# Optimization experiments

Measured on AMD Instinct MI355X. Metric: run time of the kernel, lower is better.

Reference implementation:

```python
import jax, jax.numpy as jnp
import numpy as np

N_EMBED = 1024
N_HEADS = 16
HEAD_DIM = N_EMBED // N_HEADS


def setup_inputs() -> dict:
    key = jax.random.key(0)
    ks = jax.random.split(key, 5)
    x = jax.random.normal(ks[0], (4, 2048, N_EMBED), dtype=jnp.float32)
    # Linear params (torch nn.Linear: y = x @ W.T + b); store W as [in, out]
    s = 1.0 / np.sqrt(N_EMBED)
    W_attn = jax.random.uniform(ks[1], (N_EMBED, 3 * N_EMBED), minval=-s, maxval=s, dtype=jnp.float32)
    b_attn = jax.random.uniform(ks[2], (3 * N_EMBED,), minval=-s, maxval=s, dtype=jnp.float32)
    W_proj = jax.random.uniform(ks[3], (N_EMBED, N_EMBED), minval=-s, maxval=s, dtype=jnp.float32)
    b_proj = jax.random.uniform(ks[4], (N_EMBED,), minval=-s, maxval=s, dtype=jnp.float32)
    return {"x": x, "W_attn": W_attn, "b_attn": b_attn, "W_proj": W_proj, "b_proj": b_proj}


def reference(x, W_attn, b_attn, W_proj, b_proj):
    B, L, D = x.shape
    H, Hd = N_HEADS, HEAD_DIM
    qkv = x @ W_attn + b_attn  # [B, L, 3D]
    q, k, v = jnp.split(qkv, 3, axis=-1)
    q = q.reshape(B, L, H, Hd).transpose(0, 2, 1, 3)  # [B, H, L, Hd]
    k = k.reshape(B, L, H, Hd).transpose(0, 2, 1, 3)
    v = v.reshape(B, L, H, Hd).transpose(0, 2, 1, 3)
    scores = jnp.einsum('bhqd,bhkd->bhqk', q, k) / jnp.sqrt(jnp.float32(Hd))
    causal = jnp.tril(jnp.ones((L, L), dtype=bool))
    scores = jnp.where(causal[None, None], scores, -jnp.inf)
    probs = jax.nn.softmax(scores.astype(jnp.float32), axis=-1).astype(x.dtype)
    o = jnp.einsum('bhqk,bhkd->bhqd', probs, v)  # [B, H, L, Hd]
    o = o.transpose(0, 2, 1, 3).reshape(B, L, D)
    return o @ W_proj + b_proj
```

## Files before the change

kernel.cpp:

```cpp
#include <hip/hip_runtime.h>


typedef __attribute__((ext_vector_type(8))) short short8;
typedef __attribute__((ext_vector_type(4))) short s16x4;
typedef __attribute__((ext_vector_type(4))) float f32x4;

#define DEVI __device__ __forceinline__

constexpr int NE = 1024, NH = 16, NB = 4, L = 2048;
constexpr int M = NB * L;
constexpr int KD = 1024;

DEVI unsigned f2bf(float f) {
    union { float f; unsigned u; } v; v.f = f;
    unsigned u = v.u;
    u += 0x7fffu + ((u >> 16) & 1u);
    return u >> 16;
}

typedef const __attribute__((address_space(1))) void* gas_t;
typedef __attribute__((address_space(3))) void* las_t;
DEVI void gl_lds16(const void* g, void* l) {
    __builtin_amdgcn_global_load_lds((gas_t)g, (las_t)l, 16, 0, 0);
}

__global__ void k_f32_to_bf16(const float* __restrict__ in,
                              unsigned short* __restrict__ out, int n8) {
    int i = blockIdx.x * blockDim.x + threadIdx.x;
    if (i >= n8) return;
    const float4* p = (const float4*)in + (size_t)i * 2;
    float4 a = p[0], b = p[1];
    short8 r;
    r[0] = f2bf(a.x); r[1] = f2bf(a.y); r[2] = f2bf(a.z); r[3] = f2bf(a.w);
    r[4] = f2bf(b.x); r[5] = f2bf(b.y); r[6] = f2bf(b.z); r[7] = f2bf(b.w);
    ((short8*)out)[i] = r;
}

__global__ void k_transpose_bf16(const float* __restrict__ in,
                                 unsigned short* __restrict__ out, int R, int C) {
    __shared__ float t[32][33];
    int x = blockIdx.x * 32 + threadIdx.x;
    int y0 = blockIdx.y * 32;
#pragma unroll
    for (int i = 0; i < 4; i++)
        t[threadIdx.y + 8 * i][threadIdx.x] = in[(size_t)(y0 + threadIdx.y + 8 * i) * C + x];
    __syncthreads();
    int xo = y0 + threadIdx.x;
    int yo = blockIdx.x * 32 + threadIdx.y;
#pragma unroll
    for (int i = 0; i < 4; i++)
        out[(size_t)(yo + 8 * i) * R + xo] = f2bf(t[threadIdx.x][threadIdx.y + 8 * i]);
}

template <int MODE>
__global__ __launch_bounds__(256, 2)
void k_gemm(const unsigned short* __restrict__ A,
            const unsigned short* __restrict__ Bt,
            const float* __restrict__ bias,
            unsigned short* __restrict__ Qb,
            unsigned short* __restrict__ Kb,
            unsigned short* __restrict__ Vt,
            float* __restrict__ out) {
    __shared__ alignas(16) short As[128 * 64];
    __shared__ alignas(16) short Bs[128 * 64];
    const int tid = threadIdx.x;
    const int lane = tid & 63, wid = tid >> 6;
    const int quad = lane >> 4, l16 = lane & 15;
    const int wm = (wid >> 1) * 64, wn = (wid & 1) * 64;
    const int m0 = blockIdx.y * 128;
    const int n0 = blockIdx.x * 128;

    const int srow = lane >> 3;
    const int gseg = (lane & 7) ^ srow;

    f32x4 acc[4][4] = {};

    for (int kk = 0; kk < KD; kk += 64) {
        __syncthreads();
#pragma unroll
        for (int c = 0; c < 4; c++) {
            const int rbase = c * 32 + wid * 8;
            gl_lds16(&A[(size_t)(m0 + rbase + srow) * KD + kk + gseg * 8], &As[rbase * 64]);
            gl_lds16(&Bt[(size_t)(n0 + rbase + srow) * KD + kk + gseg * 8], &Bs[rbase * 64]);
        }
        __syncthreads();
#pragma unroll
        for (int kc = 0; kc < 2; kc++) {
            short8 af[4], bf[4];
#pragma unroll
            for (int t = 0; t < 4; t++) {
                const int Ra = wm + t * 16 + l16;
                af[t] = *(const short8*)&As[Ra * 64 + (((kc * 4 + quad) ^ (Ra & 7)) * 8)];
                const int Rb = wn + t * 16 + l16;
                bf[t] = *(const short8*)&Bs[Rb * 64 + (((kc * 4 + quad) ^ (Rb & 7)) * 8)];
            }
#pragma unroll
            for (int mt = 0; mt < 4; mt++)
#pragma unroll
                for (int nt = 0; nt < 4; nt++)
                    acc[mt][nt] = __builtin_amdgcn_mfma_f32_16x16x32_bf16(
                        af[mt], bf[nt], acc[mt][nt], 0, 0, 0);
        }
    }

#pragma unroll
    for (int nt = 0; nt < 4; nt++) {
        const int n = n0 + wn + nt * 16 + l16;
        const float bv = bias[n];
        if (MODE == 0) {
            const int sel = n >> 10;
            const int h = (n & 1023) >> 6;
            const int d = n & 63;
#pragma unroll
            for (int mt = 0; mt < 4; mt++)
#pragma unroll
                for (int r = 0; r < 4; r++) {
                    const int m = m0 + wm + mt * 16 + quad * 4 + r;
                    const int b = m >> 11, l = m & 2047;
                    const int bh = b * NH + h;
                    const float v = acc[mt][nt][r] + bv;
                    if (sel == 0)      Qb[(size_t)(bh * L + l) * 64 + d] = f2bf(v * 0.125f);
                    else if (sel == 1) Kb[(size_t)(bh * L + l) * 64 + d] = f2bf(v);
                    else               Vt[(size_t)(bh * 64 + d) * L + l] = f2bf(v);
                }
        } else {
#pragma unroll
            for (int mt = 0; mt < 4; mt++)
#pragma unroll
                for (int r = 0; r < 4; r++) {
                    const int m = m0 + wm + mt * 16 + quad * 4 + r;
                    out[(size_t)m * NE + n] = acc[mt][nt][r] + bv;
                }
        }
    }
}

__global__ __launch_bounds__(256, 2)
void k_attn(const unsigned short* __restrict__ Q,
            const unsigned short* __restrict__ Kb,
            const unsigned short* __restrict__ Vt,
            unsigned short* __restrict__ O) {
    __shared__ alignas(16) short smem[16896];
    short* Ks = smem;
    short* Vs = smem + 8192;
    short* Os = smem;

    const int tid = threadIdx.x;
    const int lane = tid & 63, wid = tid >> 6;
    const int quad = lane >> 4, l16 = lane & 15;
    const int bh = blockIdx.x;
    const int pr = blockIdx.y;
    const size_t base = (size_t)bh * L * 64;
    const int b = bh >> 4, h = bh & 15;

    const int srow = lane >> 3;
    const int gsegK = (lane & 7) ^ srow;

    for (int phase = 0; phase < 2; phase++) {
        const int qb = phase ? pr : 15 - pr;
        const int q0 = qb * 128 + wid * 32;

        short8 qf[2][2];
#pragma unroll
        for (int mt = 0; mt < 2; mt++)
#pragma unroll
            for (int dc = 0; dc < 2; dc++)
                qf[mt][dc] = *(const short8*)&Q[base + (size_t)(q0 + mt * 16 + l16) * 64 + dc * 32 + quad * 8];

        f32x4 o[2][4] = {};
        float lrow[2] = {0.f, 0.f};

        for (int kt = 0; kt <= qb; kt++) {
            __syncthreads();
#pragma unroll
            for (int c = 0; c < 4; c++) {
                const int rbase = c * 32 + wid * 8;
                gl_lds16(&Kb[base + (size_t)(kt * 128 + rbase + srow) * 64 + gsegK * 8],
                         &Ks[rbase * 64]);
            }
            short8 vtmp[4];
            const int vd = lane >> 4, vseg = lane & 15;
#pragma unroll
            for (int c = 0; c < 4; c++)
                vtmp[c] = *(const short8*)&Vt[base + (size_t)(c * 16 + wid * 4 + vd) * L + kt * 128 + vseg * 8];
#pragma unroll
            for (int c = 0; c < 4; c++)
                *(short8*)&Vs[(c * 16 + wid * 4 + vd) * 136 + vseg * 8] = vtmp[c];
            __syncthreads();

            const bool diag = (kt == qb);
            const int chunks = diag ? (wid + 1) : 4;

            for (int kc = 0; kc < chunks; kc++) {
                short8 kf[2][2];
#pragma unroll
                for (int j0 = 0; j0 < 2; j0++)
#pragma unroll
                    for (int dc = 0; dc < 2; dc++) {
                        const int R = kc * 32 + j0 * 16 + l16;
                        kf[j0][dc] = *(const short8*)&Ks[R * 64 + (((dc * 4 + quad) ^ (R & 7)) * 8)];
                    }
                f32x4 st[2][2];
#pragma unroll
                for (int mt = 0; mt < 2; mt++)
#pragma unroll
                    for (int j0 = 0; j0 < 2; j0++) {
                        f32x4 z = {};
                        z = __builtin_amdgcn_mfma_f32_16x16x32_bf16(kf[j0][0], qf[mt][0], z, 0, 0, 0);
                        z = __builtin_amdgcn_mfma_f32_16x16x32_bf16(kf[j0][1], qf[mt][1], z, 0, 0, 0);
                        st[mt][j0] = z;
                    }
                const bool dm = diag && (kc == wid);
                short8 pb[2];
#pragma unroll
                for (int mt = 0; mt < 2; mt++) {
                    float sum = 0.f;
#pragma unroll
                    for (int j0 = 0; j0 < 2; j0++)
#pragma unroll
                        for (int r = 0; r < 4; r++) {
                            float pe = __expf(st[mt][j0][r]);
                            if (dm) {
                                const int krel = j0 * 16 + quad * 4 + r;
                                const int qrel = mt * 16 + l16;
                                if (krel > qrel) pe = 0.f;
                            }
                            sum += pe;
                            pb[mt][j0 * 4 + r] = (short)f2bf(pe);
                        }
                    lrow[mt] += sum;
                }
#pragma unroll
                for (int dt = 0; dt < 4; dt++) {
                    const int va = (dt * 16 + l16) * 136 + kc * 32 + quad * 4;
                    s16x4 lo = *(const s16x4*)&Vs[va];
                    s16x4 hi = *(const s16x4*)&Vs[va + 16];
                    short8 vf = __builtin_shufflevector(lo, hi, 0, 1, 2, 3, 4, 5, 6, 7);
#pragma unroll
                    for (int mt = 0; mt < 2; mt++)
                        o[mt][dt] = __builtin_amdgcn_mfma_f32_16x16x32_bf16(
                            vf, pb[mt], o[mt][dt], 0, 0, 0);
                }
            }
        }

        float inv[2];
#pragma unroll
        for (int mt = 0; mt < 2; mt++) {
            float rs = lrow[mt];
            rs += __shfl_xor(rs, 16);
            rs += __shfl_xor(rs, 32);
            inv[mt] = 1.0f / rs;
        }

        __syncthreads();
#pragma unroll
        for (int mt = 0; mt < 2; mt++) {
            const int ql = wid * 32 + mt * 16 + l16;
#pragma unroll
            for (int dt = 0; dt < 4; dt++) {
                unsigned w0 = f2bf(o[mt][dt][0] * inv[mt]) | (f2bf(o[mt][dt][1] * inv[mt]) << 16);
                unsigned w1 = f2bf(o[mt][dt][2] * inv[mt]) | (f2bf(o[mt][dt][3] * inv[mt]) << 16);
                *(uint2*)&Os[ql * 72 + dt * 16 + quad * 4] = make_uint2(w0, w1);
            }
        }
        __syncthreads();
#pragma unroll
        for (int i = 0; i < 4; i++) {
            const int id = i * 256 + tid;
            const int row = id >> 3, seg = id & 7;
            short8 v = *(const short8*)&Os[row * 72 + seg * 8];
            const int q = qb * 128 + row;
            *(short8*)&O[(size_t)(b * L + q) * NE + h * 64 + seg * 8] = v;
        }
    }
}

extern "C" void kernel_launch(void* const* d_in, const int* in_sizes, int n_in,
                              void* d_out, int out_size, void* d_ws, size_t ws_size,
                              hipStream_t stream) {
    const float* x  = (const float*)d_in[0];
    const float* Wa = (const float*)d_in[1];
    const float* ba = (const float*)d_in[2];
    const float* Wp = (const float*)d_in[3];
    const float* bp = (const float*)d_in[4];
    float* out = (float*)d_out;

    char* ws = (char*)d_ws;
    unsigned short* xb  = (unsigned short*)(ws);
    unsigned short* WaT = (unsigned short*)(ws + (16u << 20));
    unsigned short* WpT = (unsigned short*)(ws + (22u << 20));
    unsigned short* Qb  = (unsigned short*)(ws + (24u << 20));
    unsigned short* Kb  = (unsigned short*)(ws + (40u << 20));
    unsigned short* Vt  = (unsigned short*)(ws + (56u << 20));

    k_f32_to_bf16<<<(M * NE / 8 + 255) / 256, 256, 0, stream>>>(x, xb, M * NE / 8);
    k_transpose_bf16<<<dim3(3 * NE / 32, NE / 32), dim3(32, 8), 0, stream>>>(Wa, WaT, NE, 3 * NE);
    k_transpose_bf16<<<dim3(NE / 32, NE / 32), dim3(32, 8), 0, stream>>>(Wp, WpT, NE, NE);

    k_gemm<0><<<dim3(3 * NE / 128, M / 128), 256, 0, stream>>>(xb, WaT, ba, Qb, Kb, Vt, nullptr);

    unsigned short* Ob = xb;
    k_attn<<<dim3(NB * NH, 8), 256, 0, stream>>>(Qb, Kb, Vt, Ob);

    k_gemm<1><<<dim3(NE / 128, M / 128), 256, 0, stream>>>(Ob, WpT, bp, nullptr, nullptr, nullptr, out);
}
```

Measured before the change: 267.7 us.

## Split attention to one q-block per workgroup, async swizzled V loads

```diff
diff --git a/kernel.cpp b/kernel.cpp
--- a/kernel.cpp
+++ b/kernel.cpp
@@ -16,6 +16,10 @@
     unsigned u = v.u;
     u += 0x7fffu + ((u >> 16) & 1u);
     return u >> 16;
+}
+DEVI unsigned pack_bf2(float lo, float hi) {
+    union { float f; unsigned u; } a, b; a.f = lo; b.f = hi;
+    return ((a.u + 0x8000u) >> 16) | ((b.u + 0x8000u) & 0xffff0000u);
 }
 
 typedef const __attribute__((address_space(1))) void* gas_t;
@@ -53,7 +57,7 @@
 }
 
 template <int MODE>
-__global__ __launch_bounds__(256, 2)
+__global__ __launch_bounds__(256, 4)
 void k_gemm(const unsigned short* __restrict__ A,
             const unsigned short* __restrict__ Bt,
             const float* __restrict__ bias,
@@ -135,12 +139,12 @@
     }
 }
 
-__global__ __launch_bounds__(256, 2)
+__global__ __launch_bounds__(256, 4)
 void k_attn(const unsigned short* __restrict__ Q,
             const unsigned short* __restrict__ Kb,
             const unsigned short* __restrict__ Vt,
             unsigned short* __restrict__ O) {
-    __shared__ alignas(16) short smem[16896];
+    __shared__ alignas(16) short smem[16384];
     short* Ks = smem;
     short* Vs = smem + 8192;
     short* Os = smem;
@@ -149,130 +153,136 @@
     const int lane = tid & 63, wid = tid >> 6;
     const int quad = lane >> 4, l16 = lane & 15;
     const int bh = blockIdx.x;
-    const int pr = blockIdx.y;
+    const int qb = 15 - (int)blockIdx.y;
+    const int q0 = qb * 128 + wid * 32;
     const size_t base = (size_t)bh * L * 64;
     const int b = bh >> 4, h = bh & 15;
 
-    const int srow = lane >> 3;
-    const int gsegK = (lane & 7) ^ srow;
-
-    for (int phase = 0; phase < 2; phase++) {
-        const int qb = phase ? pr : 15 - pr;
-        const int q0 = qb * 128 + wid * 32;
-
-        short8 qf[2][2];
-#pragma unroll
-        for (int mt = 0; mt < 2; mt++)
-#pragma unroll
-            for (int dc = 0; dc < 2; dc++)
-                qf[mt][dc] = *(const short8*)&Q[base + (size_t)(q0 + mt * 16 + l16) * 64 + dc * 32 + quad * 8];
-
-        f32x4 o[2][4] = {};
-        float lrow[2] = {0.f, 0.f};
-
-        for (int kt = 0; kt <= qb; kt++) {
-            __syncthreads();
-#pragma unroll
-            for (int c = 0; c < 4; c++) {
-                const int rbase = c * 32 + wid * 8;
-                gl_lds16(&Kb[base + (size_t)(kt * 128 + rbase + srow) * 64 + gsegK * 8],
-                         &Ks[rbase * 64]);
+    const int srowK = lane >> 3;
+    const int gsegK = (lane & 7) ^ srowK;
+    const int vrow_off = (lane >> 4);
+    const int vseg = lane & 15;
+
+    short8 qf[2][2];
+#pragma unroll
+    for (int mt = 0; mt < 2; mt++)
+#pragma unroll
+        for (int dc = 0; dc < 2; dc++)
+            qf[mt][dc] = *(const short8*)&Q[base + (size_t)(q0 + mt * 16 + l16) * 64 + dc * 32 + quad * 8];
+
+    f32x4 o[2][4] = {};
+    float lrow[2] = {0.f, 0.f};
+
+    for (int kt = 0; kt <= qb; kt++) {
+        __syncthreads();
+#pragma unroll
+        for (int c = 0; c < 4; c++) {
+            const int rbase = c * 32 + wid * 8;
+            gl_lds16(&Kb[base + (size_t)(kt * 128 + rbase + srowK) * 64 + gsegK * 8],
+                     &Ks[rbase * 64]);
+        }
+#pragma unroll
+        for (int c = 0; c < 4; c++) {
+            const int rbase = c * 16 + wid * 4;
+            const int row = rbase + vrow_off;
+            const int gs = vseg ^ (row & 15);
+            gl_lds16(&Vt[base + (size_t)row * L + kt * 128 + gs * 8], &Vs[rbase * 128]);
+        }
+        __syncthreads();
+
+        const bool diag = (kt == qb);
+        const int chunks = diag ? (wid + 1) : 4;
+
+        for (int kc = 0; kc < chunks; kc++) {
+            short8 kf[2][2];
+#pragma unroll
+            for (int j0 = 0; j0 < 2; j0++)
+#pragma unroll
+                for (int dc = 0; dc < 2; dc++) {
+                    const int R = kc * 32 + j0 * 16 + l16;
+                    kf[j0][dc] = *(const short8*)&Ks[R * 64 + (((dc * 4 + quad) ^ (R & 7)) * 8)];
+                }
+            f32x4 st[2][2];
+#pragma unroll
+            for (int mt = 0; mt < 2; mt++)
+#pragma unroll
+                for (int j0 = 0; j0 < 2; j0++) {
+                    f32x4 z = {};
+                    z = __builtin_amdgcn_mfma_f32_16x16x32_bf16(kf[j0][0], qf[mt][0], z, 0, 0, 0);
+                    z = __builtin_amdgcn_mfma_f32_16x16x32_bf16(kf[j0][1], qf[mt][1], z, 0, 0, 0);
+                    st[mt][j0] = z;
+                }
+            const bool dm = diag && (kc == wid);
+            short8 pb[2];
+#pragma unroll
+            for (int mt = 0; mt < 2; mt++) {
+                float pe[8];
+                float sum = 0.f;
+#pragma unroll
+                for (int j0 = 0; j0 < 2; j0++)
+#pragma unroll
+                    for (int r = 0; r < 4; r++) {
+                        float p = __expf(st[mt][j0][r]);
+                        if (dm) {
+                            const int krel = j0 * 16 + quad * 4 + r;
+                            const int qrel = mt * 16 + l16;
+                            if (krel > qrel) p = 0.f;
+                        }
+                        sum += p;
+                        pe[j0 * 4 + r] = p;
+                    }
+                lrow[mt] += sum;
+#pragma unroll
+                for (int w = 0; w < 4; w++) {
+                    unsigned pk = pack_bf2(pe[2 * w], pe[2 * w + 1]);
+                    pb[mt][2 * w] = (short)(pk & 0xffff);
+                    pb[mt][2 * w + 1] = (short)(pk >> 16);
+                }
             }
-            short8 vtmp[4];
-            const int vd = lane >> 4, vseg = lane & 15;
-#pragma unroll
-            for (int c = 0; c < 4; c++)
-                vtmp[c] = *(const short8*)&Vt[base + (size_t)(c * 16 + wid * 4 + vd) * L + kt * 128 + vseg * 8];
-#pragma unroll
-            for (int c = 0; c < 4; c++)
-                *(short8*)&Vs[(c * 16 + wid * 4 + vd) * 136 + vseg * 8] = vtmp[c];
-            __syncthreads();
-
-            const bool diag = (kt == qb);
-            const int chunks = diag ? (wid + 1) : 4;
-
-            for (int kc = 0; kc < chunks; kc++) {
-                short8 kf[2][2];
-#pragma unroll
-                for (int j0 = 0; j0 < 2; j0++)
-#pragma unroll
-                    for (int dc = 0; dc < 2; dc++) {
-                        const int R = kc * 32 + j0 * 16 + l16;
-                        kf[j0][dc] = *(const short8*)&Ks[R * 64 + (((dc * 4 + quad) ^ (R & 7)) * 8)];
-                    }
-                f32x4 st[2][2];
+#pragma unroll
+            for (int dt = 0; dt < 4; dt++) {
+                const int R2 = dt * 16 + l16;
+                const int s16a = kc * 4 + (quad >> 1);
+                const int off = (quad & 1) * 4;
+                s16x4 lo = *(const s16x4*)&Vs[R2 * 128 + ((s16a ^ l16) * 8) + off];
+                s16x4 hi = *(const s16x4*)&Vs[R2 * 128 + (((s16a + 2) ^ l16) * 8) + off];
+                short8 vf = __builtin_shufflevector(lo, hi, 0, 1, 2, 3, 4, 5, 6, 7);
 #pragma unroll
                 for (int mt = 0; mt < 2; mt++)
-#pragma unroll
-                    for (int j0 = 0; j0 < 2; j0++) {
-                        f32x4 z = {};
-                        z = __builtin_amdgcn_mfma_f32_16x16x32_bf16(kf[j0][0], qf[mt][0], z, 0, 0, 0);
-                        z = __builtin_amdgcn_mfma_f32_16x16x32_bf16(kf[j0][1], qf[mt][1], z, 0, 0, 0);
-                        st[mt][j0] = z;
-                    }
-                const bool dm = diag && (kc == wid);
-                short8 pb[2];
-#pragma unroll
-                for (int mt = 0; mt < 2; mt++) {
-                    float sum = 0.f;
-#pragma unroll
-                    for (int j0 = 0; j0 < 2; j0++)
-#pragma unroll
-                        for (int r = 0; r < 4; r++) {
-                            float pe = __expf(st[mt][j0][r]);
-                            if (dm) {
-                                const int krel = j0 * 16 + quad * 4 + r;
-                                const int qrel = mt * 16 + l16;
-                                if (krel > qrel) pe = 0.f;
-                            }
-                            sum += pe;
-                            pb[mt][j0 * 4 + r] = (short)f2bf(pe);
-                        }
-                    lrow[mt] += sum;
-                }
-#pragma unroll
-                for (int dt = 0; dt < 4; dt++) {
-                    const int va = (dt * 16 + l16) * 136 + kc * 32 + quad * 4;
-                    s16x4 lo = *(const s16x4*)&Vs[va];
-                    s16x4 hi = *(const s16x4*)&Vs[va + 16];
-                    short8 vf = __builtin_shufflevector(lo, hi, 0, 1, 2, 3, 4, 5, 6, 7);
-#pragma unroll
-                    for (int mt = 0; mt < 2; mt++)
-                        o[mt][dt] = __builtin_amdgcn_mfma_f32_16x16x32_bf16(
-                            vf, pb[mt], o[mt][dt], 0, 0, 0);
-                }
+                    o[mt][dt] = __builtin_amdgcn_mfma_f32_16x16x32_bf16(
+                        vf, pb[mt], o[mt][dt], 0, 0, 0);
             }
         }
-
-        float inv[2];
-#pragma unroll
-        for (int mt = 0; mt < 2; mt++) {
-            float rs = lrow[mt];
-            rs += __shfl_xor(rs, 16);
-            rs += __shfl_xor(rs, 32);
-            inv[mt] = 1.0f / rs;
-        }
-
-        __syncthreads();
-#pragma unroll
-        for (int mt = 0; mt < 2; mt++) {
-            const int ql = wid * 32 + mt * 16 + l16;
-#pragma unroll
-            for (int dt = 0; dt < 4; dt++) {
-                unsigned w0 = f2bf(o[mt][dt][0] * inv[mt]) | (f2bf(o[mt][dt][1] * inv[mt]) << 16);
-                unsigned w1 = f2bf(o[mt][dt][2] * inv[mt]) | (f2bf(o[mt][dt][3] * inv[mt]) << 16);
-                *(uint2*)&Os[ql * 72 + dt * 16 + quad * 4] = make_uint2(w0, w1);
-            }
-        }
-        __syncthreads();
-#pragma unroll
-        for (int i = 0; i < 4; i++) {
-            const int id = i * 256 + tid;
-            const int row = id >> 3, seg = id & 7;
-            short8 v = *(const short8*)&Os[row * 72 + seg * 8];
-            const int q = qb * 128 + row;
-            *(short8*)&O[(size_t)(b * L + q) * NE + h * 64 + seg * 8] = v;
-        }
+    }
+
+    float inv[2];
+#pragma unroll
+    for (int mt = 0; mt < 2; mt++) {
+        float rs = lrow[mt];
+        rs += __shfl_xor(rs, 16);
+        rs += __shfl_xor(rs, 32);
+        inv[mt] = 1.0f / rs;
+    }
+
+    __syncthreads();
+#pragma unroll
+    for (int mt = 0; mt < 2; mt++) {
+        const int ql = wid * 32 + mt * 16 + l16;
+#pragma unroll
+        for (int dt = 0; dt < 4; dt++) {
+            unsigned w0 = f2bf(o[mt][dt][0] * inv[mt]) | (f2bf(o[mt][dt][1] * inv[mt]) << 16);
+            unsigned w1 = f2bf(o[mt][dt][2] * inv[mt]) | (f2bf(o[mt][dt][3] * inv[mt]) << 16);
+            *(uint2*)&Os[ql * 72 + dt * 16 + quad * 4] = make_uint2(w0, w1);
+        }
+    }
+    __syncthreads();
+#pragma unroll
+    for (int i = 0; i < 4; i++) {
+        const int id = i * 256 + tid;
+        const int row = id >> 3, seg = id & 7;
+        short8 v = *(const short8*)&Os[row * 72 + seg * 8];
+        const int q = qb * 128 + row;
+        *(short8*)&O[(size_t)(b * L + q) * NE + h * 64 + seg * 8] = v;
     }
 }
 
@@ -301,7 +311,7 @@
     k_gemm<0><<<dim3(3 * NE / 128, M / 128), 256, 0, stream>>>(xb, WaT, ba, Qb, Kb, Vt, nullptr);
 
     unsigned short* Ob = xb;
-    k_attn<<<dim3(NB * NH, 8), 256, 0, stream>>>(Qb, Kb, Vt, Ob);
+    k_attn<<<dim3(NB * NH, 16), 256, 0, stream>>>(Qb, Kb, Vt, Ob);
 
     k_gemm<1><<<dim3(NE / 128, M / 128), 256, 0, stream>>>(Ob, WpT, bp, nullptr, nullptr, nullptr, out);
 }
```

New measurement: 259.9 us. 1.03x faster.
